# Performance work log

Hardware: AMD Instinct MI355X
Metric: run time of the kernel (lower is better)

The kernel has to match this reference:

```python
import jax, jax.numpy as jnp
import numpy as np

B, N_TOTAL, IN_CH, N_SUB, E, OUT_CH = 4096, 500, 8, 77, 400, 2
EPS = 1e-12


def _glorot(key, shape, scale=0.05):
    return jax.random.normal(key, shape, dtype=jnp.float32) * scale


def setup_inputs() -> dict:
    key = jax.random.key(0)
    ks = jax.random.split(key, 16)
    x = jax.random.normal(ks[0], (B, N_TOTAL, IN_CH), dtype=jnp.float32)
    n_id = jax.random.randint(ks[1], (N_SUB,), 0, N_TOTAL)
    edge_index = jax.random.randint(ks[2], (2, E), 0, N_SUB)
    return {
        "x": x, "n_id": n_id, "edge_index": edge_index,
        # SAGEConv weights: concat doubles the input dim
        "W1": _glorot(ks[3], (2 * IN_CH, 64)), "b1": jnp.zeros((64,), jnp.float32),
        "W2": _glorot(ks[4], (2 * 64, 256)),   "b2": jnp.zeros((256,), jnp.float32),
        "W3": _glorot(ks[5], (2 * 256, 512)),  "b3": jnp.zeros((512,), jnp.float32),
        # MLP head
        "L1w": _glorot(ks[6], (512 * N_SUB, 1024), 0.01), "L1b": jnp.zeros((1024,), jnp.float32),
        "L2w": _glorot(ks[7], (1024, 218)), "L2b": jnp.zeros((218,), jnp.float32),
        "L3w": _glorot(ks[8], (218, OUT_CH)), "L3b": jnp.zeros((OUT_CH,), jnp.float32),
    }


def sage_conv(x, edge_index, W, b):
    # x: [B, N_SUB, C]; edge_index: [2, E], local ids in [0, N_SUB)
    # PyG<=1.3 SAGEConv: remove self loops, add self loops, mean aggregate,
    # concat [x, aggr], linear, L2 normalize.
    src, dst = edge_index[0], edge_index[1]
    valid = (src != dst)
    vmask = valid.astype(x.dtype)
    msgs = x[:, src, :] * vmask[None, :, None]                       # [B, E, C]
    seg = jax.vmap(lambda m: jax.ops.segment_sum(m, dst, num_segments=N_SUB))(msgs)
    counts = jax.ops.segment_sum(vmask, dst, num_segments=N_SUB)     # [N_SUB]
    aggr = (seg + x) / (counts + 1.0)[None, :, None]                 # self loop included
    h = jnp.concatenate([x, aggr], axis=-1) @ W + b
    norm = jnp.linalg.norm(h, axis=-1, keepdims=True)
    return h / jnp.maximum(norm, EPS)


def reference(x, n_id, edge_index, W1, b1, W2, b2, W3, b3,
              L1w, L1b, L2w, L2b, L3w, L3b):
    xt = x[:, n_id, :]                                               # [B, 77, 8]
    xt = jax.nn.relu(sage_conv(xt, edge_index, W1, b1))              # [B, 77, 64]
    xt = jax.nn.relu(sage_conv(xt, edge_index, W2, b2))              # [B, 77, 256]
    xt = jax.nn.relu(sage_conv(xt, edge_index, W3, b3))              # [B, 77, 512]
    xt = xt.reshape(xt.shape[0], -1)                                 # [B, 39424]
    xt = jax.nn.relu(xt @ L1w + L1b)
    xt = jax.nn.relu(xt @ L2w + L2b)
    return xt @ L3w + L3b                                            # [B, 2]
```

## Files before the change

### kernel.cpp

```cpp
#include <hip/hip_runtime.h>
#include <hip/hip_bf16.h>
#include <stdint.h>

typedef unsigned short u16;
typedef __attribute__((ext_vector_type(8))) short bf16x8_t;
typedef __attribute__((ext_vector_type(4))) float f32x4_t;

#define B_SZ   4096
#define N_TOT  500
#define IN_CH  8
#define NS     77
#define NE     400
#define L2_OUT 218

#define AS1C(p) ((const __attribute__((address_space(1))) void*)(p))
#define AS3(p)  ((__attribute__((address_space(3))) void*)(p))

__device__ inline u16 f2b(float f) {
  union { float f; uint32_t u; } v; v.f = f;
  uint32_t r = v.u + 0x7FFFu + ((v.u >> 16) & 1u);
  return (u16)(r >> 16);
}
__device__ inline float b2f(u16 h) {
  union { uint32_t u; float f; } v; v.u = ((uint32_t)h) << 16; return v.f;
}
__device__ inline uint32_t pk(float a, float b) {
  return (uint32_t)f2b(a) | ((uint32_t)f2b(b) << 16);
}

__global__ void k_setup(const int* __restrict__ ei, int* __restrict__ coff,
                        int* __restrict__ csrc, float* __restrict__ inv) {
  __shared__ int s_src[NE], s_dst[NE];
  __shared__ int s_cnt[NS], s_off[NS + 1];
  const int t = threadIdx.x;
  for (int e = t; e < NE; e += 128) { s_src[e] = ei[e]; s_dst[e] = ei[NE + e]; }
  __syncthreads();
  if (t < NS) {
    int c = 0;
    for (int e = 0; e < NE; ++e) c += (s_dst[e] == t && s_src[e] != t) ? 1 : 0;
    s_cnt[t] = c;
  }
  __syncthreads();
  if (t == 0) {
    int acc = 0;
    for (int i = 0; i < NS; ++i) { s_off[i] = acc; acc += s_cnt[i]; }
    s_off[NS] = acc;
  }
  __syncthreads();
  if (t < NS) {
    int o = s_off[t];
    for (int e = 0; e < NE; ++e)
      if (s_dst[e] == t && s_src[e] != t) csrc[o++] = s_src[e];
    coff[t] = s_off[t];
    inv[t] = 1.0f / (float)(s_cnt[t] + 1);
  }
  if (t == 0) coff[NS] = s_off[NS];
}

__global__ void k_wt(const float* __restrict__ W, u16* __restrict__ Wt,
                     int K, int Nsrc, int Ndst) {
  __shared__ float t[32][33];
  int nk = K / 32;
  int bk = blockIdx.x % nk, bn = blockIdx.x / nk;
  int r = threadIdx.x >> 3, c4 = (threadIdx.x & 7) * 4;
  int gn = bn * 32 + c4;
  const float* src = &W[(size_t)(bk * 32 + r) * Nsrc + gn];
  if (gn + 3 < Nsrc) {
    float4 v = *(const float4*)src;
    t[r][c4] = v.x; t[r][c4+1] = v.y; t[r][c4+2] = v.z; t[r][c4+3] = v.w;
  } else {
    #pragma unroll
    for (int j = 0; j < 4; ++j) t[r][c4 + j] = (gn + j < Nsrc) ? src[j] : 0.f;
  }
  __syncthreads();
  ushort4 o;
  o.x = f2b(t[c4+0][r]); o.y = f2b(t[c4+1][r]);
  o.z = f2b(t[c4+2][r]); o.w = f2b(t[c4+3][r]);
  *(ushort4*)&Wt[(size_t)(bn * 32 + r) * K + bk * 32 + c4] = o;
}

__global__ __launch_bounds__(256)
void k_front(const float* __restrict__ x, const int* __restrict__ nid,
             const float* __restrict__ W1, const float* __restrict__ b1,
             const int* __restrict__ coff, const int* __restrict__ csrc,
             const float* __restrict__ invc,
             u16* __restrict__ h1, u16* __restrict__ ag1) {
  __shared__ float Ws[16 * 64];
  __shared__ float bs[64];
  __shared__ float xs[NS * 8];
  __shared__ float ac[NS * 16];
  __shared__ u16  hn[NS * 64];
  __shared__ int soff[NS + 1];
  __shared__ int ssrc[NE];
  __shared__ float sinv[NS];
  __shared__ int snid[NS];
  const int b = blockIdx.x, t = threadIdx.x;

  ((float4*)Ws)[t] = ((const float4*)W1)[t];
  if (t < 64) bs[t] = b1[t];
  if (t < NS) { snid[t] = nid[t]; sinv[t] = invc[t]; }
  if (t < NS + 1) soff[t] = coff[t];
  for (int i = t; i < NE; i += 256) ssrc[i] = csrc[i];
  __syncthreads();

  if (t < 2 * NS) {
    int i = t >> 1, p = t & 1;
    float4 v = *(const float4*)(x + ((size_t)b * N_TOT + snid[i]) * IN_CH + p * 4);
    *(float4*)&xs[i * 8 + p * 4] = v;
  }
  __syncthreads();

  for (int idx = t; idx < NS * 8; idx += 256) {
    int i = idx >> 3, c = idx & 7;
    float s = xs[i * 8 + c];
    ac[i * 16 + c] = s;
    for (int e = soff[i]; e < soff[i + 1]; ++e) s += xs[ssrc[e] * 8 + c];
    ac[i * 16 + 8 + c] = s * sinv[i];
  }
  __syncthreads();

  const int w = t >> 6, lane = t & 63;
  for (int i = w; i < NS; i += 4) {
    float acc = bs[lane];
    #pragma unroll
    for (int k = 0; k < 16; ++k) acc += ac[i * 16 + k] * Ws[k * 64 + lane];
    float ss = acc * acc;
    #pragma unroll
    for (int d = 1; d < 64; d <<= 1) ss += __shfl_xor(ss, d);
    float rn = 1.0f / fmaxf(sqrtf(ss), 1e-12f);
    u16 hv = f2b(fmaxf(acc * rn, 0.f));
    hn[i * 64 + lane] = hv;
    h1[((size_t)b * NS + i) * 64 + lane] = hv;
  }
  __syncthreads();
  for (int i = w; i < NS; i += 4) {
    float s = b2f(hn[i * 64 + lane]);
    for (int e = soff[i]; e < soff[i + 1]; ++e) s += b2f(hn[ssrc[e] * 64 + lane]);
    ag1[((size_t)b * NS + i) * 64 + lane] = f2b(s * sinv[i]);
  }
}

template<int C>
__global__ __launch_bounds__(256)
void k_norm_aggr(u16* __restrict__ h, u16* __restrict__ ag,
                 const int* __restrict__ coff, const int* __restrict__ csrc,
                 const float* __restrict__ invc) {
  __shared__ u16 sh[NS * C];
  __shared__ int soff[NS + 1];
  __shared__ int ssrc[NE];
  __shared__ float sinv[NS];
  const int b = blockIdx.x, t = threadIdx.x;
  const ushort4* hb4 = (const ushort4*)(h + (size_t)b * NS * C);
  ushort4* sh4 = (ushort4*)sh;
  for (int i4 = t; i4 < NS * C / 4; i4 += 256) sh4[i4] = hb4[i4];
  for (int i = t; i < NS + 1; i += 256) soff[i] = coff[i];
  for (int i = t; i < NE; i += 256) ssrc[i] = csrc[i];
  for (int i = t; i < NS; i += 256) sinv[i] = invc[i];
  __syncthreads();
  const int w = t >> 6, lane = t & 63;
  constexpr int PER = C / 64;
  ushort4* hb4o = (ushort4*)(h + (size_t)b * NS * C);
  for (int i = w; i < NS; i += 4) {
    float v[PER]; float ss = 0.f;
    #pragma unroll
    for (int p = 0; p < PER / 4; ++p) {
      ushort4 r = *(ushort4*)&sh[i * C + lane * PER + p * 4];
      v[p*4+0] = b2f(r.x); v[p*4+1] = b2f(r.y); v[p*4+2] = b2f(r.z); v[p*4+3] = b2f(r.w);
    }
    #pragma unroll
    for (int p = 0; p < PER; ++p) ss += v[p] * v[p];
    #pragma unroll
    for (int d = 1; d < 64; d <<= 1) ss += __shfl_xor(ss, d);
    float rn = 1.0f / fmaxf(sqrtf(ss), 1e-12f);
    #pragma unroll
    for (int p = 0; p < PER / 4; ++p) {
      ushort4 o;
      o.x = f2b(fmaxf(v[p*4+0] * rn, 0.f)); o.y = f2b(fmaxf(v[p*4+1] * rn, 0.f));
      o.z = f2b(fmaxf(v[p*4+2] * rn, 0.f)); o.w = f2b(fmaxf(v[p*4+3] * rn, 0.f));
      *(ushort4*)&sh[i * C + lane * PER + p * 4] = o;
      hb4o[(i * C + lane * PER + p * 4) / 4] = o;
    }
  }
  __syncthreads();
  ushort4* ab4 = (ushort4*)(ag + (size_t)b * NS * C);
  for (int i = w; i < NS; i += 4) {
    #pragma unroll
    for (int p = 0; p < PER / 4; ++p) {
      int c0 = lane * PER + p * 4;
      ushort4 sv = *(ushort4*)&sh[i * C + c0];
      float s0 = b2f(sv.x), s1 = b2f(sv.y), s2 = b2f(sv.z), s3 = b2f(sv.w);
      for (int e = soff[i]; e < soff[i + 1]; ++e) {
        ushort4 nv = *(ushort4*)&sh[ssrc[e] * C + c0];
        s0 += b2f(nv.x); s1 += b2f(nv.y); s2 += b2f(nv.z); s3 += b2f(nv.w);
      }
      float iv = sinv[i];
      ushort4 o; o.x = f2b(s0 * iv); o.y = f2b(s1 * iv); o.z = f2b(s2 * iv); o.w = f2b(s3 * iv);
      ab4[(i * C + c0) / 4] = o;
    }
  }
}

template<int C>
__global__ void k_normrelu(u16* __restrict__ h) {
  static_assert(C == 512, "specialized for C=512");
  const int row = blockIdx.x * 4 + (threadIdx.x >> 6);
  const int lane = threadIdx.x & 63;
  u16* hr = h + (size_t)row * C + lane * 8;
  uint4 r = *(const uint4*)hr;
  float v[8];
  v[0]=b2f((u16)(r.x & 0xffff)); v[1]=b2f((u16)(r.x >> 16));
  v[2]=b2f((u16)(r.y & 0xffff)); v[3]=b2f((u16)(r.y >> 16));
  v[4]=b2f((u16)(r.z & 0xffff)); v[5]=b2f((u16)(r.z >> 16));
  v[6]=b2f((u16)(r.w & 0xffff)); v[7]=b2f((u16)(r.w >> 16));
  float ss = 0.f;
  #pragma unroll
  for (int j = 0; j < 8; ++j) ss += v[j] * v[j];
  #pragma unroll
  for (int d = 1; d < 64; d <<= 1) ss += __shfl_xor(ss, d);
  float rn = 1.0f / fmaxf(sqrtf(ss), 1e-12f);
  #pragma unroll
  for (int j = 0; j < 8; ++j) v[j] = fmaxf(v[j] * rn, 0.f);
  uint4 o;
  o.x = pk(v[0], v[1]); o.y = pk(v[2], v[3]);
  o.z = pk(v[4], v[5]); o.w = pk(v[6], v[7]);
  *(uint4*)hr = o;
}

template<int MODE, bool CONCAT>
__global__ __launch_bounds__(256)
void k_mfma(const u16* __restrict__ A, const u16* __restrict__ A2,
            const u16* __restrict__ Bt, const float* __restrict__ bias,
            void* __restrict__ Cv, int N, int K, int CIN,
            int kPerSplit, int Mtot) {
  __shared__ u16 As[2][128 * 32];
  __shared__ u16 Bs[2][128 * 32];
  const int t = threadIdx.x;
  const int gx = gridDim.x, gy = gridDim.y;
  const int nwg = gx * gy;
  const int orig = blockIdx.y * gx + blockIdx.x;
  const int q = nwg >> 3, r8 = nwg & 7;
  const int xcd = orig & 7, jj = orig >> 3;
  const int swzb = (xcd < r8 ? xcd * (q + 1) : r8 * (q + 1) + (xcd - r8) * q) + jj;
  const int mt_i = swzb / gy, nt_i = swzb - mt_i * gy;
  const int row0 = mt_i * 128, col0 = nt_i * 128;
  const int split = blockIdx.z;
  const int kbeg = split * kPerSplit;
  const int w = t >> 6, l = t & 63;
  const int wm = w >> 1, wn = w & 1;
  const int lr = l & 15, ls = l >> 4;
  const int s_row = t >> 2;
  const int s_c = ((t & 3) ^ ((t >> 3) & 3)) * 8;
  const int lsw = (ls ^ ((lr >> 1) & 3)) * 8;

  f32x4_t acc[4][4];
  #pragma unroll
  for (int i = 0; i < 4; ++i)
    #pragma unroll
    for (int j = 0; j < 4; ++j) acc[i][j] = (f32x4_t){0.f, 0.f, 0.f, 0.f};

  auto stage = [&](int buf, int k0) {
    const u16* abase; int astride, koff;
    if constexpr (CONCAT) {
      astride = CIN;
      if (k0 < CIN) { abase = A; koff = k0; } else { abase = A2; koff = k0 - CIN; }
    } else { abase = A; astride = K; koff = k0; }
    const u16* ga0 = abase + (size_t)(row0 + s_row) * astride + koff + s_c;
    const u16* ga1 = abase + (size_t)(row0 + 64 + s_row) * astride + koff + s_c;
    u16* la = &As[buf][w * 512];
    __builtin_amdgcn_global_load_lds(AS1C(ga0), AS3(la), 16, 0, 0);
    __builtin_amdgcn_global_load_lds(AS1C(ga1), AS3(la + 2048), 16, 0, 0);
    const u16* gb0 = Bt + (size_t)(col0 + s_row) * K + k0 + s_c;
    const u16* gb1 = Bt + (size_t)(col0 + 64 + s_row) * K + k0 + s_c;
    u16* lb = &Bs[buf][w * 512];
    __builtin_amdgcn_global_load_lds(AS1C(gb0), AS3(lb), 16, 0, 0);
    __builtin_amdgcn_global_load_lds(AS1C(gb1), AS3(lb + 2048), 16, 0, 0);
  };

  const int nsteps = kPerSplit / 32;
  stage(0, kbeg);
  __syncthreads();
  for (int s = 0; s < nsteps; ++s) {
    const int buf = s & 1;
    if (s + 1 < nsteps) stage(buf ^ 1, kbeg + (s + 1) * 32);
    bf16x8_t af[4], bfr[4];
    #pragma unroll
    for (int f = 0; f < 4; ++f) {
      af[f]  = *(const bf16x8_t*)&As[buf][(wm * 64 + f * 16 + lr) * 32 + lsw];
      bfr[f] = *(const bf16x8_t*)&Bs[buf][(wn * 64 + f * 16 + lr) * 32 + lsw];
    }
    #pragma unroll
    for (int i = 0; i < 4; ++i)
      #pragma unroll
      for (int j = 0; j < 4; ++j)
        acc[i][j] = __builtin_amdgcn_mfma_f32_16x16x32_bf16(af[i], bfr[j], acc[i][j], 0, 0, 0);
    __syncthreads();
  }

  #pragma unroll
  for (int j = 0; j < 4; ++j) {
    const int c = col0 + wn * 64 + j * 16 + lr;
    float bv = 0.f;
    if constexpr (MODE == 0) bv = bias[c];
    #pragma unroll
    for (int i = 0; i < 4; ++i) {
      const int r0 = row0 + wm * 64 + i * 16 + ls * 4;
      if constexpr (MODE == 0) {
        u16* C = (u16*)Cv;
        #pragma unroll
        for (int rr = 0; rr < 4; ++rr)
          C[(size_t)(r0 + rr) * N + c] = f2b(acc[i][j][rr] + bv);
      } else {
        float* P = (float*)Cv + (size_t)split * Mtot * N;
        #pragma unroll
        for (int rr = 0; rr < 4; ++rr)
          P[(size_t)(r0 + rr) * N + c] = acc[i][j][rr];
      }
    }
  }
}

__global__ void k_red4(const float* __restrict__ P, const float* __restrict__ bias,
                       u16* __restrict__ y, int MN) {
  int i = blockIdx.x * 256 + threadIdx.x;
  if (i * 4 >= MN) return;
  const float4* p = (const float4*)P;
  int stride = MN / 4;
  float4 a = p[i], b = p[i + stride], c = p[i + 2 * stride], d = p[i + 3 * stride];
  float4 bv = *(const float4*)&bias[(i * 4) & 1023];
  ushort4 o;
  o.x = f2b(fmaxf(a.x + b.x + c.x + d.x + bv.x, 0.f));
  o.y = f2b(fmaxf(a.y + b.y + c.y + d.y + bv.y, 0.f));
  o.z = f2b(fmaxf(a.z + b.z + c.z + d.z + bv.z, 0.f));
  o.w = f2b(fmaxf(a.w + b.w + c.w + d.w + bv.w, 0.f));
  *(ushort4*)&y[i * 4] = o;
}

__global__ void k_tail(const float* __restrict__ P, const float* __restrict__ L2bias,
                       const float* __restrict__ w, const float* __restrict__ b,
                       float* __restrict__ out, int nb) {
  const int row = blockIdx.x * 4 + (threadIdx.x >> 6);
  const int lane = threadIdx.x & 63;
  if (row >= nb) return;
  const int MN = nb * 256;
  float s0 = 0.f, s1 = 0.f;
  #pragma unroll
  for (int j = 0; j < 4; ++j) {
    int col = lane + 64 * j;
    if (col < L2_OUT) {
      int idx = row * 256 + col;
      float v = P[idx] + P[idx + MN] + P[idx + 2 * MN] + P[idx + 3 * MN];
      v = fmaxf(v + L2bias[col], 0.f);
      s0 += v * w[col * 2];
      s1 += v * w[col * 2 + 1];
    }
  }
  #pragma unroll
  for (int d = 1; d < 64; d <<= 1) { s0 += __shfl_xor(s0, d); s1 += __shfl_xor(s1, d); }
  if (lane == 0) { out[(size_t)row * 2] = s0 + b[0]; out[(size_t)row * 2 + 1] = s1 + b[1]; }
}

extern "C" void kernel_launch(void* const* d_in, const int* in_sizes, int n_in,
                              void* d_out, int out_size, void* d_ws, size_t ws_size,
                              hipStream_t stream) {
  const float* x   = (const float*)d_in[0];
  const int*   nid = (const int*)d_in[1];
  const int*   ei  = (const int*)d_in[2];
  const float* W1  = (const float*)d_in[3];  const float* b1 = (const float*)d_in[4];
  const float* W2  = (const float*)d_in[5];  const float* b2 = (const float*)d_in[6];
  const float* W3  = (const float*)d_in[7];  const float* b3 = (const float*)d_in[8];
  const float* L1w = (const float*)d_in[9];  const float* L1b = (const float*)d_in[10];
  const float* L2w = (const float*)d_in[11]; const float* L2b = (const float*)d_in[12];
  const float* L3w = (const float*)d_in[13]; const float* L3b = (const float*)d_in[14];
  float* out = (float*)d_out;

  char* ws = (char*)d_ws;
  u16* Wt2  = (u16*)ws;
  u16* Wt3  = (u16*)(ws + 65536);
  u16* WtL1 = (u16*)(ws + 589824);
  u16* WtL2 = (u16*)(ws + 81330176);
  size_t WOFF = 81854464;
  int*   coff = (int*)(ws + WOFF);
  int*   csrc = coff + 80;
  float* invc = (float*)(csrc + 400);
  size_t CHUNK0 = WOFF + 4096;

  int Bc = 4096;
  while (Bc > 128 && CHUNK0 + (size_t)Bc * 157696 > ws_size) Bc >>= 1;

  char* r1 = ws + CHUNK0;
  char* r2 = r1 + (size_t)Bc * 39424;
  char* r3 = r2 + (size_t)Bc * 39424;

  k_setup<<<1, 128, 0, stream>>>(ei, coff, csrc, invc);
  k_wt<<<(128/32)*(256/32),    256, 0, stream>>>(W2,  Wt2,  128,   256,  256);
  k_wt<<<(512/32)*(512/32),    256, 0, stream>>>(W3,  Wt3,  512,   512,  512);
  k_wt<<<(39424/32)*(1024/32), 256, 0, stream>>>(L1w, WtL1, 39424, 1024, 1024);
  k_wt<<<(1024/32)*(256/32),   256, 0, stream>>>(L2w, WtL2, 1024,  218,  256);

  for (int b0 = 0; b0 < B_SZ; b0 += Bc) {
    const int nb = Bc;
    const int rows = nb * NS;
    const int mt = rows / 128;
    u16* h1  = (u16*)r2;
    u16* ag1 = (u16*)r3;
    u16* h2  = (u16*)r1;
    u16* ag2 = (u16*)r2;
    u16* h3  = (u16*)r3;
    u16* y1b = (u16*)r1;
    float* Pc  = (float*)(r1 + (size_t)nb * 4096);
    float* Pc2 = (float*)(r1 + (size_t)nb * 4096);
    const float* xb = x + (size_t)b0 * N_TOT * IN_CH;

    k_front<<<nb, 256, 0, stream>>>(xb, nid, W1, b1, coff, csrc, invc, h1, ag1);

    k_mfma<0, true><<<dim3(mt, 2, 1), 256, 0, stream>>>(
        h1, ag1, Wt2, b2, h2, 256, 128, 64, 128, rows);
    k_norm_aggr<256><<<nb, 256, 0, stream>>>(h2, ag2, coff, csrc, invc);

    k_mfma<0, true><<<dim3(mt, 4, 1), 256, 0, stream>>>(
        h2, ag2, Wt3, b3, h3, 512, 512, 256, 512, rows);
    k_normrelu<512><<<rows / 4, 256, 0, stream>>>(h3);

    k_mfma<1, false><<<dim3(nb / 128, 8, 4), 256, 0, stream>>>(
        h3, nullptr, WtL1, nullptr, Pc, 1024, 39424, 0, 9856, nb);
    k_red4<<<nb, 256, 0, stream>>>(Pc, L1b, y1b, nb * 1024);

    k_mfma<1, false><<<dim3(nb / 128, 2, 4), 256, 0, stream>>>(
        y1b, nullptr, WtL2, nullptr, Pc2, 256, 1024, 0, 256, nb);
    k_tail<<<(nb + 3) / 4, 256, 0, stream>>>(Pc2, L2b, L3w, L3b, out + (size_t)b0 * 2, nb);
  }
}
```

Baseline: 1.300 ms.

## Add 256x256 8-wave MFMA GEMM with interleaved staging for layer3 and L1

Introduces a new 512-thread GEMM kernel with 256x256 output tiles, double-buffered LDS filled via direct global-to-LDS loads that are interleaved with MFMA quadrants, XOR-swizzled LDS reads, s_setprio around MFMA bursts and an XCD-aware block remap. It replaces the 128-tile kernel for the SAGE layer-3 GEMM and the large L1 split-K GEMM, aiming to raise arithmetic intensity and overlap loads with compute. The minimum batch chunk rises to 256 so the tile divides evenly. Larger LDS use (128KB) and register pressure may limit occupancy.

```diff
diff --git a/kernel.cpp b/kernel.cpp
--- a/kernel.cpp
+++ b/kernel.cpp
@@ -319,6 +319,187 @@
   }
 }
 
+template<int MODE, bool CONCAT>
+__global__ __launch_bounds__(512, 2)
+void k_m8(const u16* __restrict__ A, const u16* __restrict__ A2,
+          const u16* __restrict__ Bt, const float* __restrict__ bias,
+          void* __restrict__ Cv, int N, int K, int CIN,
+          int kPerSplit, int Mtot) {
+  __shared__ u16 Asl[2][256 * 64];
+  __shared__ u16 Bsl[2][256 * 64];
+  const int t = threadIdx.x;
+  const int gx = gridDim.x, gy = gridDim.y;
+  const int nwg = gx * gy;
+  const int orig = blockIdx.y * gx + blockIdx.x;
+  const int q = nwg >> 3, r8 = nwg & 7;
+  const int xcd = orig & 7, jj = orig >> 3;
+  const int swzb = (xcd < r8 ? xcd * (q + 1) : r8 * (q + 1) + (xcd - r8) * q) + jj;
+  const int mt_i = swzb / gy, nt_i = swzb - mt_i * gy;
+  const int row0 = mt_i * 256, col0 = nt_i * 256;
+  const int split = blockIdx.z;
+  const int kbeg = split * kPerSplit;
+  const int w = t >> 6, l = t & 63;
+  const int wm = w >> 2, wn = w & 3;
+  const int lr = l & 15, ls = l >> 4;
+  const int lr7 = lr & 7;
+  const int srw = w * 8 + (l >> 3);
+  const int scl = ((l & 7) ^ (l >> 3)) * 8;
+
+  f32x4_t acc[8][4];
+  #pragma unroll
+  for (int i = 0; i < 8; ++i)
+    #pragma unroll
+    for (int j = 0; j < 4; ++j) acc[i][j] = (f32x4_t){0.f, 0.f, 0.f, 0.f};
+
+  bf16x8_t Ar[8][2];
+  bf16x8_t Br[4][2];
+
+  auto stagePart = [&](int tile, int part) {
+    const int bb = tile & 1;
+    const int k0 = kbeg + tile * 64;
+    if (part < 2) {
+      const u16* abase; int astride, koff;
+      if constexpr (CONCAT) {
+        astride = CIN;
+        if (k0 < CIN) { abase = A; koff = k0; } else { abase = A2; koff = k0 - CIN; }
+      } else { abase = A; astride = K; koff = k0; }
+      const int rb = part * 128;
+      const u16* g0 = abase + (size_t)(row0 + rb + srw) * astride + koff + scl;
+      const u16* g1 = abase + (size_t)(row0 + rb + 64 + srw) * astride + koff + scl;
+      u16* d = &Asl[bb][rb * 64 + w * 512];
+      __builtin_amdgcn_global_load_lds(AS1C(g0), AS3(d), 16, 0, 0);
+      __builtin_amdgcn_global_load_lds(AS1C(g1), AS3(d + 4096), 16, 0, 0);
+    } else {
+      const int rb = (part - 2) * 128;
+      const u16* g0 = Bt + (size_t)(col0 + rb + srw) * K + k0 + scl;
+      const u16* g1 = Bt + (size_t)(col0 + rb + 64 + srw) * K + k0 + scl;
+      u16* d = &Bsl[bb][rb * 64 + w * 512];
+      __builtin_amdgcn_global_load_lds(AS1C(g0), AS3(d), 16, 0, 0);
+      __builtin_amdgcn_global_load_lds(AS1C(g1), AS3(d + 4096), 16, 0, 0);
+    }
+  };
+
+#define RD_ALO(BB)                                                            \
+  _Pragma("unroll")                                                           \
+  for (int mf = 0; mf < 4; ++mf) {                                            \
+    _Pragma("unroll")                                                         \
+    for (int kh = 0; kh < 2; ++kh)                                            \
+      Ar[mf][kh] = *(const bf16x8_t*)&Asl[BB][(wm * 128 + mf * 16 + lr) * 64  \
+                                             + ((kh * 4 + ls) ^ lr7) * 8];    \
+  }
+#define RD_AHI(BB)                                                            \
+  _Pragma("unroll")                                                           \
+  for (int mf = 0; mf < 4; ++mf) {                                            \
+    _Pragma("unroll")                                                         \
+    for (int kh = 0; kh < 2; ++kh)                                            \
+      Ar[4 + mf][kh] = *(const bf16x8_t*)&Asl[BB][(wm * 128 + 64 + mf * 16 + lr) * 64 \
+                                                 + ((kh * 4 + ls) ^ lr7) * 8];\
+  }
+#define RD_BLO(BB)                                                            \
+  _Pragma("unroll")                                                           \
+  for (int nf = 0; nf < 2; ++nf) {                                            \
+    _Pragma("unroll")                                                         \
+    for (int kh = 0; kh < 2; ++kh)                                            \
+      Br[nf][kh] = *(const bf16x8_t*)&Bsl[BB][(wn * 64 + nf * 16 + lr) * 64   \
+                                             + ((kh * 4 + ls) ^ lr7) * 8];    \
+  }
+#define RD_BHI(BB)                                                            \
+  _Pragma("unroll")                                                           \
+  for (int nf = 0; nf < 2; ++nf) {                                            \
+    _Pragma("unroll")                                                         \
+    for (int kh = 0; kh < 2; ++kh)                                            \
+      Br[2 + nf][kh] = *(const bf16x8_t*)&Bsl[BB][(wn * 64 + 32 + nf * 16 + lr) * 64 \
+                                                 + ((kh * 4 + ls) ^ lr7) * 8];\
+  }
+#define DO_QUAD(QM, QN)                                                       \
+  __builtin_amdgcn_s_setprio(1);                                              \
+  {                                                                           \
+    _Pragma("unroll")                                                         \
+    for (int mf = 0; mf < 4; ++mf) {                                          \
+      _Pragma("unroll")                                                       \
+      for (int nf = 0; nf < 2; ++nf) {                                        \
+        _Pragma("unroll")                                                     \
+        for (int kh = 0; kh < 2; ++kh)                                        \
+          acc[(QM) * 4 + mf][(QN) * 2 + nf] =                                 \
+              __builtin_amdgcn_mfma_f32_16x16x32_bf16(                        \
+                  Ar[(QM) * 4 + mf][kh], Br[(QN) * 2 + nf][kh],               \
+                  acc[(QM) * 4 + mf][(QN) * 2 + nf], 0, 0, 0);                \
+      }                                                                       \
+    }                                                                         \
+  }                                                                           \
+  __builtin_amdgcn_s_setprio(0);
+
+  const int NT = kPerSplit / 64;
+  stagePart(0, 0); stagePart(0, 1); stagePart(0, 2); stagePart(0, 3);
+  stagePart(1, 0);
+
+  const int NI = NT / 2;
+  for (int i = 0; i < NI; ++i) {
+    const int tO = 2 * i + 1;
+    const bool s2 = (2 * i + 2) < NT;
+    asm volatile("s_waitcnt vmcnt(2)" ::: "memory");
+    __builtin_amdgcn_s_barrier();
+    asm volatile("" ::: "memory");
+    stagePart(tO, 1);
+    RD_ALO(0) RD_BLO(0)
+    DO_QUAD(0, 0)
+    stagePart(tO, 2);
+    RD_AHI(0)
+    DO_QUAD(1, 0)
+    stagePart(tO, 3);
+    RD_BHI(0)
+    DO_QUAD(0, 1)
+    __builtin_amdgcn_s_barrier();
+    asm volatile("" ::: "memory");
+    if (s2) stagePart(2 * i + 2, 0);
+    DO_QUAD(1, 1)
+    if (s2) { asm volatile("s_waitcnt vmcnt(2)" ::: "memory"); }
+    else    { asm volatile("s_waitcnt vmcnt(0)" ::: "memory"); }
+    __builtin_amdgcn_s_barrier();
+    asm volatile("" ::: "memory");
+    if (s2) stagePart(2 * i + 2, 1);
+    RD_ALO(1) RD_BLO(1)
+    DO_QUAD(0, 0)
+    if (s2) stagePart(2 * i + 2, 2);
+    RD_AHI(1)
+    DO_QUAD(1, 0)
+    if (s2) stagePart(2 * i + 2, 3);
+    RD_BHI(1)
+    DO_QUAD(0, 1)
+    __builtin_amdgcn_s_barrier();
+    asm volatile("" ::: "memory");
+    if (2 * i + 3 < NT) stagePart(2 * i + 3, 0);
+    DO_QUAD(1, 1)
+  }
+
+  #pragma unroll
+  for (int j = 0; j < 4; ++j) {
+    const int c = col0 + wn * 64 + j * 16 + lr;
+    float bv = 0.f;
+    if constexpr (MODE == 0) bv = bias[c];
+    #pragma unroll
+    for (int i = 0; i < 8; ++i) {
+      const int r0 = row0 + wm * 128 + i * 16 + ls * 4;
+      if constexpr (MODE == 0) {
+        u16* C = (u16*)Cv;
+        #pragma unroll
+        for (int rr = 0; rr < 4; ++rr)
+          C[(size_t)(r0 + rr) * N + c] = f2b(acc[i][j][rr] + bv);
+      } else {
+        float* P = (float*)Cv + (size_t)split * Mtot * N;
+        #pragma unroll
+        for (int rr = 0; rr < 4; ++rr)
+          P[(size_t)(r0 + rr) * N + c] = acc[i][j][rr];
+      }
+    }
+  }
+#undef RD_ALO
+#undef RD_AHI
+#undef RD_BLO
+#undef RD_BHI
+#undef DO_QUAD
+}
+
 __global__ void k_red4(const float* __restrict__ P, const float* __restrict__ bias,
                        u16* __restrict__ y, int MN) {
   int i = blockIdx.x * 256 + threadIdx.x;
@@ -385,7 +566,7 @@
   size_t CHUNK0 = WOFF + 4096;
 
   int Bc = 4096;
-  while (Bc > 128 && CHUNK0 + (size_t)Bc * 157696 > ws_size) Bc >>= 1;
+  while (Bc > 256 && CHUNK0 + (size_t)Bc * 157696 > ws_size) Bc >>= 1;
 
   char* r1 = ws + CHUNK0;
   char* r2 = r1 + (size_t)Bc * 39424;
@@ -417,11 +598,11 @@
         h1, ag1, Wt2, b2, h2, 256, 128, 64, 128, rows);
     k_norm_aggr<256><<<nb, 256, 0, stream>>>(h2, ag2, coff, csrc, invc);
 
-    k_mfma<0, true><<<dim3(mt, 4, 1), 256, 0, stream>>>(
+    k_m8<0, true><<<dim3(rows / 256, 2, 1), 512, 0, stream>>>(
         h2, ag2, Wt3, b3, h3, 512, 512, 256, 512, rows);
     k_normrelu<512><<<rows / 4, 256, 0, stream>>>(h3);
 
-    k_mfma<1, false><<<dim3(nb / 128, 8, 4), 256, 0, stream>>>(
+    k_m8<1, false><<<dim3(nb / 256, 4, 4), 512, 0, stream>>>(
         h3, nullptr, WtL1, nullptr, Pc, 1024, 39424, 0, 9856, nb);
     k_red4<<<nb, 256, 0, stream>>>(Pc, L1b, y1b, nb * 1024);
 
```

Measured after the change: 1.364 ms. 1.05x slower.
